# Optimization experiments

Hardware: AMD Instinct MI355X
Metric: run time of the kernel (lower is better)

Reference implementation:

```python
import jax, jax.numpy as jnp
import numpy as np

N = 100000   # nodes
E = 1600000  # edges
IN, HID, OUT = 128, 256, 64


def _glorot(key, shape):
    fan_in, fan_out = shape[1], shape[0]
    lim = (6.0 / (fan_in + fan_out)) ** 0.5
    return jax.random.uniform(key, shape, jnp.float32, -lim, lim)


def setup_inputs() -> dict:
    key = jax.random.key(0)
    ks = jax.random.split(key, 8)
    x = jax.random.normal(ks[0], (N, IN), jnp.float32)
    edge_index = jax.random.randint(ks[1], (2, E), 0, N, jnp.int64)
    # SAGEConv params: lin_l (neighbor path, has bias), lin_r (root path, no bias)
    return {
        "x": x,
        "edge_index": edge_index,
        "W1_l": _glorot(ks[2], (HID, IN)),
        "b1": jnp.zeros((HID,), jnp.float32),
        "W1_r": _glorot(ks[3], (HID, IN)),
        "W2_l": _glorot(ks[4], (OUT, HID)),
        "b2": jnp.zeros((OUT,), jnp.float32),
        "W2_r": _glorot(ks[5], (OUT, HID)),
    }


def _sage_conv(x, src, dst, W_l, b, W_r):
    # mean aggregation of neighbor features at destination nodes
    msg = x[src]                                             # [E, d] gather
    agg = jax.ops.segment_sum(msg, dst, num_segments=N)      # [N, d]
    cnt = jax.ops.segment_sum(jnp.ones((src.shape[0],), jnp.float32), dst,
                              num_segments=N)                # [N]
    mean = agg / jnp.maximum(cnt, 1.0)[:, None]
    return mean @ W_l.T + b + x @ W_r.T


def reference(x, edge_index, W1_l, b1, W1_r, W2_l, b2, W2_r):
    src, dst = edge_index[0], edge_index[1]
    h = jax.nn.relu(_sage_conv(x, src, dst, W1_l, b1, W1_r))
    # dropout is identity in eval mode
    return _sage_conv(h, src, dst, W2_l, b2, W2_r)
```

## Files before the change

kernel.cpp:

```cpp
#include <hip/hip_runtime.h>
#include <hip/hip_bf16.h>

#define NNODE 100000
#define NEDGE 1600000
#define NBBLK 512
#define CHUNK (NEDGE / NBBLK)
#define NB2 ((NNODE + 1023) >> 10)

typedef __attribute__((ext_vector_type(8))) short bf16x8;
typedef __attribute__((ext_vector_type(4))) float f32x4;
typedef __attribute__((ext_vector_type(2))) float f32x2;

__device__ __forceinline__ unsigned short f2bf(float f){
  unsigned u = __float_as_uint(f);
  u += 0x7fffu + ((u >> 16) & 1u);
  return (unsigned short)(u >> 16);
}
__device__ __forceinline__ unsigned pk2(float a, float b){
  return (unsigned)f2bf(a) | ((unsigned)f2bf(b) << 16);
}
__device__ __forceinline__ float bflo(unsigned v){ return __uint_as_float(v << 16); }
__device__ __forceinline__ float bfhi(unsigned v){ return __uint_as_float(v & 0xffff0000u); }

__global__ __launch_bounds__(256) void k_hist(const int* __restrict__ dst,
                                              unsigned* __restrict__ gh){
  __shared__ unsigned h[NB2];
  for (int t = threadIdx.x; t < NB2; t += 256) h[t] = 0;
  __syncthreads();
  int base = blockIdx.x * CHUNK;
  for (int j = threadIdx.x; j < CHUNK; j += 256)
    atomicAdd(&h[dst[base + j] >> 10], 1u);
  __syncthreads();
  for (int t = threadIdx.x; t < NB2; t += 256) gh[blockIdx.x * NB2 + t] = h[t];
}

__global__ __launch_bounds__(512) void k_scan512(const unsigned* __restrict__ gh,
                                                 unsigned* __restrict__ gbase,
                                                 unsigned* __restrict__ btot){
  int b = blockIdx.x, t = threadIdx.x;
  int lane = t & 63, wv = t >> 6;
  unsigned v = gh[t * NB2 + b];
  unsigned s = v;
  #pragma unroll
  for (int off = 1; off < 64; off <<= 1){
    unsigned u = __shfl_up(s, off, 64);
    if (lane >= off) s += u;
  }
  __shared__ unsigned wsum[8];
  if (lane == 63) wsum[wv] = s;
  __syncthreads();
  unsigned woff = 0;
  for (int w = 0; w < wv; ++w) woff += wsum[w];
  gbase[t * NB2 + b] = woff + s - v;
  if (t == 511) btot[b] = woff + s;
}

__global__ __launch_bounds__(128) void k_scanb(const unsigned* __restrict__ btot,
                                               unsigned* __restrict__ bbase,
                                               unsigned* __restrict__ rowptr){
  __shared__ unsigned buf[128];
  int tid = threadIdx.x;
  unsigned v = (tid < NB2) ? btot[tid] : 0u;
  buf[tid] = v;
  __syncthreads();
  #pragma unroll
  for (int off = 1; off < 128; off <<= 1){
    unsigned t = (tid >= off) ? buf[tid - off] : 0u;
    __syncthreads();
    buf[tid] += t;
    __syncthreads();
  }
  if (tid < NB2) bbase[tid] = buf[tid] - v;
  if (tid == 0){ bbase[NB2] = NEDGE; rowptr[NNODE] = NEDGE; }
}

__global__ __launch_bounds__(256) void k_binscat(const int* __restrict__ src,
                                                 const int* __restrict__ dst,
                                                 const unsigned* __restrict__ gbase,
                                                 const unsigned* __restrict__ bbase,
                                                 unsigned* __restrict__ pairs){
  __shared__ unsigned cur[NB2];
  for (int t = threadIdx.x; t < NB2; t += 256)
    cur[t] = bbase[t] + gbase[blockIdx.x * NB2 + t];
  __syncthreads();
  int base = blockIdx.x * CHUNK;
  for (int j = threadIdx.x; j < CHUNK; j += 256){
    int s = src[base + j], d = dst[base + j];
    unsigned p = atomicAdd(&cur[d >> 10], 1u);
    pairs[p] = ((unsigned)s << 10) | (unsigned)(d & 1023);
  }
}

__global__ __launch_bounds__(1024) void k_buildcsr(const unsigned* __restrict__ bbase,
                                                   const unsigned* __restrict__ pairs,
                                                   unsigned* __restrict__ rowptr,
                                                   unsigned* __restrict__ col){
  __shared__ unsigned hist[1024];
  __shared__ unsigned wsum[16];
  const int b = blockIdx.x, tid = threadIdx.x;
  const int lane = tid & 63, wv = tid >> 6;
  const unsigned e0 = bbase[b], e1 = bbase[b + 1];
  const int nb0 = b << 10;
  hist[tid] = 0;
  __syncthreads();
  for (unsigned j = e0 + tid; j < e1; j += 1024)
    atomicAdd(&hist[pairs[j] & 1023u], 1u);
  __syncthreads();
  unsigned v = hist[tid];
  unsigned s = v;
  #pragma unroll
  for (int off = 1; off < 64; off <<= 1){
    unsigned u = __shfl_up(s, off, 64);
    if (lane >= off) s += u;
  }
  if (lane == 63) wsum[wv] = s;
  __syncthreads();
  unsigned woff = 0;
  for (int w = 0; w < wv; ++w) woff += wsum[w];
  unsigned gpos = e0 + woff + s - v;
  if (nb0 + tid < NNODE) rowptr[nb0 + tid] = gpos;
  __syncthreads();
  hist[tid] = gpos;
  __syncthreads();
  for (unsigned j = e0 + tid; j < e1; j += 1024){
    unsigned e = pairs[j];
    unsigned p = atomicAdd(&hist[e & 1023u], 1u);
    col[p] = e >> 10;
  }
}

__global__ void k_xcvt(const float* __restrict__ x, unsigned* __restrict__ A1u,
                       unsigned* __restrict__ x8u){
  int i = blockIdx.x * 256 + threadIdx.x;
  if (i >= NNODE * 32) return;
  float4 v = ((const float4*)x)[i];
  int e = i * 4;
  int row = e >> 7, c = e & 127;
  unsigned* d = A1u + (size_t)row * 128 + 64 + (c >> 1);
  d[0] = pk2(v.x, v.y);
  d[1] = pk2(v.z, v.w);
  unsigned p = (unsigned)__builtin_amdgcn_cvt_pk_fp8_f32(v.x, v.y, 0, false);
  p = (unsigned)__builtin_amdgcn_cvt_pk_fp8_f32(v.z, v.w, (int)p, true);
  x8u[(size_t)row * 32 + (c >> 2)] = p;
}

__global__ void k_wcvt1(const float* __restrict__ W1l, const float* __restrict__ W1r,
                        unsigned short* __restrict__ Bwt1){
  int i = blockIdx.x * 256 + threadIdx.x;
  if (i >= 256 * 256) return;
  int n = i >> 8, k = i & 255;
  float v = (k < 128) ? W1l[n * 128 + k] : W1r[n * 128 + (k - 128)];
  Bwt1[i] = f2bf(v);
}

__global__ void k_wcvt2(const float* __restrict__ W2l, const float* __restrict__ W2r,
                        unsigned short* __restrict__ Bwt2){
  int i = blockIdx.x * 256 + threadIdx.x;
  if (i >= 128 * 256) return;
  int n = i >> 8, k = i & 255;
  float v = (n < 64) ? W2l[n * 256 + k] : W2r[(n - 64) * 256 + k];
  Bwt2[i] = f2bf(v);
}

__global__ void k_zcvt(const unsigned* __restrict__ zru, unsigned* __restrict__ z8u){
  int i = blockIdx.x * 256 + threadIdx.x;
  if (i >= NNODE * 16) return;
  int node = i >> 4, g = i & 15;
  uint2 v = ((const uint2*)(zru + (size_t)node * 64))[g];
  unsigned p = (unsigned)__builtin_amdgcn_cvt_pk_fp8_f32(bflo(v.x), bfhi(v.x), 0, false);
  p = (unsigned)__builtin_amdgcn_cvt_pk_fp8_f32(bflo(v.y), bfhi(v.y), (int)p, true);
  z8u[(size_t)node * 16 + g] = p;
}

__global__ __launch_bounds__(256) void k_agg1(const unsigned* __restrict__ rowptr,
                                              const unsigned* __restrict__ col,
                                              const unsigned* __restrict__ x8u,
                                              unsigned* __restrict__ A1u){
  int gw = (blockIdx.x * 256 + threadIdx.x) >> 6;
  int lane = threadIdx.x & 63;
  if (gw >= NNODE) return;
  unsigned s0 = rowptr[gw], s1 = rowptr[gw + 1];
  const int sel = lane >> 4, u = lane & 15;
  const uint2* x82 = (const uint2*)x8u;
  float a0=0.f,a1=0.f,a2=0.f,a3=0.f,a4=0.f,a5=0.f,a6=0.f,a7=0.f;
  unsigned j = s0;
  for (; j + 7 < s1; j += 8){
    unsigned ca = col[j + sel], cb = col[j + 4 + sel];
    uint2 va = x82[(size_t)ca * 16 + u];
    uint2 vb = x82[(size_t)cb * 16 + u];
    f32x2 p;
    p = __builtin_amdgcn_cvt_pk_f32_fp8((int)va.x, false); a0+=p.x; a1+=p.y;
    p = __builtin_amdgcn_cvt_pk_f32_fp8((int)va.x, true ); a2+=p.x; a3+=p.y;
    p = __builtin_amdgcn_cvt_pk_f32_fp8((int)va.y, false); a4+=p.x; a5+=p.y;
    p = __builtin_amdgcn_cvt_pk_f32_fp8((int)va.y, true ); a6+=p.x; a7+=p.y;
    p = __builtin_amdgcn_cvt_pk_f32_fp8((int)vb.x, false); a0+=p.x; a1+=p.y;
    p = __builtin_amdgcn_cvt_pk_f32_fp8((int)vb.x, true ); a2+=p.x; a3+=p.y;
    p = __builtin_amdgcn_cvt_pk_f32_fp8((int)vb.y, false); a4+=p.x; a5+=p.y;
    p = __builtin_amdgcn_cvt_pk_f32_fp8((int)vb.y, true ); a6+=p.x; a7+=p.y;
  }
  for (; j + 3 < s1; j += 4){
    unsigned ca = col[j + sel];
    uint2 va = x82[(size_t)ca * 16 + u];
    f32x2 p;
    p = __builtin_amdgcn_cvt_pk_f32_fp8((int)va.x, false); a0+=p.x; a1+=p.y;
    p = __builtin_amdgcn_cvt_pk_f32_fp8((int)va.x, true ); a2+=p.x; a3+=p.y;
    p = __builtin_amdgcn_cvt_pk_f32_fp8((int)va.y, false); a4+=p.x; a5+=p.y;
    p = __builtin_amdgcn_cvt_pk_f32_fp8((int)va.y, true ); a6+=p.x; a7+=p.y;
  }
  int rem = (int)(s1 - j);
  if (sel < rem){
    unsigned ca = col[j + sel];
    uint2 va = x82[(size_t)ca * 16 + u];
    f32x2 p;
    p = __builtin_amdgcn_cvt_pk_f32_fp8((int)va.x, false); a0+=p.x; a1+=p.y;
    p = __builtin_amdgcn_cvt_pk_f32_fp8((int)va.x, true ); a2+=p.x; a3+=p.y;
    p = __builtin_amdgcn_cvt_pk_f32_fp8((int)va.y, false); a4+=p.x; a5+=p.y;
    p = __builtin_amdgcn_cvt_pk_f32_fp8((int)va.y, true ); a6+=p.x; a7+=p.y;
  }
  a0 += __shfl_xor(a0, 16, 64); a1 += __shfl_xor(a1, 16, 64);
  a2 += __shfl_xor(a2, 16, 64); a3 += __shfl_xor(a3, 16, 64);
  a4 += __shfl_xor(a4, 16, 64); a5 += __shfl_xor(a5, 16, 64);
  a6 += __shfl_xor(a6, 16, 64); a7 += __shfl_xor(a7, 16, 64);
  a0 += __shfl_xor(a0, 32, 64); a1 += __shfl_xor(a1, 32, 64);
  a2 += __shfl_xor(a2, 32, 64); a3 += __shfl_xor(a3, 32, 64);
  a4 += __shfl_xor(a4, 32, 64); a5 += __shfl_xor(a5, 32, 64);
  a6 += __shfl_xor(a6, 32, 64); a7 += __shfl_xor(a7, 32, 64);
  if (lane < 16){
    float inv = 1.f / fmaxf((float)(s1 - s0), 1.f);
    uint4 w;
    w.x = pk2(a0 * inv, a1 * inv);
    w.y = pk2(a2 * inv, a3 * inv);
    w.z = pk2(a4 * inv, a5 * inv);
    w.w = pk2(a6 * inv, a7 * inv);
    *(uint4*)(A1u + (size_t)gw * 128 + 4 * lane) = w;
  }
}

template<int BN, bool RELU, bool BIAS>
__global__ __launch_bounds__(256) void k_gemm(const unsigned short* __restrict__ A,
                                              const unsigned short* __restrict__ B,
                                              const float* __restrict__ bias,
                                              unsigned short* __restrict__ C,
                                              int nrows){
  constexpr int NF = BN / 64;
  __shared__ unsigned short a_t[64 * 64];
  __shared__ unsigned short b_t[BN * 64];
  const int tid = threadIdx.x, wave = tid >> 6, lane = tid & 63;
  const int row0 = blockIdx.x * 64;
  char* ab = (char*)a_t;
  char* bb = (char*)b_t;

  f32x4 acc[4][NF];
  #pragma unroll
  for (int m = 0; m < 4; ++m)
    #pragma unroll
    for (int n = 0; n < NF; ++n)
      acc[m][n] = (f32x4){0.f, 0.f, 0.f, 0.f};

  for (int kt = 0; kt < 4; ++kt){
    {
      int r = tid >> 2;
      int gr = row0 + r; if (gr > nrows - 1) gr = nrows - 1;
      const uint4* s4 = (const uint4*)(A + (size_t)gr * 256 + kt * 64);
      int c0 = (tid & 3) * 2;
      uint4 v0 = s4[c0], v1 = s4[c0 + 1];
      *(uint4*)(ab + r * 128 + ((c0 * 16) ^ ((r & 7) << 4))) = v0;
      *(uint4*)(ab + r * 128 + (((c0 + 1) * 16) ^ ((r & 7) << 4))) = v1;
    }
    {
      constexpr int CPT = BN / 32;
      #pragma unroll
      for (int c = 0; c < CPT; ++c){
        int gc = tid * CPT + c;
        int n = gc >> 3, ck = gc & 7;
        uint4 v = ((const uint4*)(B + (size_t)n * 256 + kt * 64))[ck];
        *(uint4*)(bb + n * 128 + ((ck * 16) ^ ((n & 7) << 4))) = v;
      }
    }
    __syncthreads();
    #pragma unroll
    for (int kk = 0; kk < 2; ++kk){
      int k2 = (kk * 32 + ((lane >> 4) * 8)) * 2;
      bf16x8 af[4];
      #pragma unroll
      for (int m = 0; m < 4; ++m){
        int rr = m * 16 + (lane & 15);
        af[m] = *(const bf16x8*)(ab + rr * 128 + (k2 ^ ((rr & 7) << 4)));
      }
      #pragma unroll
      for (int n = 0; n < NF; ++n){
        int cc = wave * (16 * NF) + n * 16 + (lane & 15);
        bf16x8 bfv = *(const bf16x8*)(bb + cc * 128 + (k2 ^ ((cc & 7) << 4)));
        #pragma unroll
        for (int m = 0; m < 4; ++m)
          acc[m][n] = __builtin_amdgcn_mfma_f32_16x16x32_bf16(af[m], bfv, acc[m][n], 0, 0, 0);
      }
    }
    __syncthreads();
  }
  #pragma unroll
  for (int m = 0; m < 4; ++m){
    int rbase = row0 + m * 16 + ((lane >> 4) << 2);
    #pragma unroll
    for (int r = 0; r < 4; ++r){
      if (rbase + r < nrows){
        #pragma unroll
        for (int n = 0; n < NF; ++n){
          int cc = wave * (16 * NF) + n * 16 + (lane & 15);
          float v = acc[m][n][r];
          if (BIAS) v += bias[cc];
          if (RELU) v = fmaxf(v, 0.f);
          C[(size_t)(rbase + r) * BN + cc] = f2bf(v);
        }
      }
    }
  }
}

__global__ __launch_bounds__(256) void k_agg2(const unsigned* __restrict__ rowptr,
                                              const unsigned* __restrict__ col,
                                              const unsigned* __restrict__ z8u,
                                              const unsigned* __restrict__ zru,
                                              const float* __restrict__ b2,
                                              float* __restrict__ out){
  int gw = (blockIdx.x * 256 + threadIdx.x) >> 6;
  int lane = threadIdx.x & 63;
  if (gw >= NNODE) return;
  unsigned s0 = rowptr[gw], s1 = rowptr[gw + 1];
  const int sel = lane >> 4, u = lane & 15;
  float a0=0.f,a1=0.f,a2=0.f,a3=0.f;
  unsigned j = s0;
  for (; j + 7 < s1; j += 8){
    unsigned ca = col[j + sel], cb = col[j + 4 + sel];
    unsigned va = z8u[(size_t)ca * 16 + u];
    unsigned vb = z8u[(size_t)cb * 16 + u];
    f32x2 p;
    p = __builtin_amdgcn_cvt_pk_f32_fp8((int)va, false); a0+=p.x; a1+=p.y;
    p = __builtin_amdgcn_cvt_pk_f32_fp8((int)va, true ); a2+=p.x; a3+=p.y;
    p = __builtin_amdgcn_cvt_pk_f32_fp8((int)vb, false); a0+=p.x; a1+=p.y;
    p = __builtin_amdgcn_cvt_pk_f32_fp8((int)vb, true ); a2+=p.x; a3+=p.y;
  }
  for (; j + 3 < s1; j += 4){
    unsigned ca = col[j + sel];
    unsigned va = z8u[(size_t)ca * 16 + u];
    f32x2 p;
    p = __builtin_amdgcn_cvt_pk_f32_fp8((int)va, false); a0+=p.x; a1+=p.y;
    p = __builtin_amdgcn_cvt_pk_f32_fp8((int)va, true ); a2+=p.x; a3+=p.y;
  }
  int rem = (int)(s1 - j);
  if (sel < rem){
    unsigned ca = col[j + sel];
    unsigned va = z8u[(size_t)ca * 16 + u];
    f32x2 p;
    p = __builtin_amdgcn_cvt_pk_f32_fp8((int)va, false); a0+=p.x; a1+=p.y;
    p = __builtin_amdgcn_cvt_pk_f32_fp8((int)va, true ); a2+=p.x; a3+=p.y;
  }
  a0 += __shfl_xor(a0, 16, 64); a1 += __shfl_xor(a1, 16, 64);
  a2 += __shfl_xor(a2, 16, 64); a3 += __shfl_xor(a3, 16, 64);
  a0 += __shfl_xor(a0, 32, 64); a1 += __shfl_xor(a1, 32, 64);
  a2 += __shfl_xor(a2, 32, 64); a3 += __shfl_xor(a3, 32, 64);
  if (lane < 16){
    float inv = 1.f / fmaxf((float)(s1 - s0), 1.f);
    uint2 rv = ((const uint2*)(zru + (size_t)gw * 64 + 32))[lane];
    float4 bv = ((const float4*)b2)[lane];
    float4 res;
    res.x = a0 * inv + bflo(rv.x) + bv.x;
    res.y = a1 * inv + bfhi(rv.x) + bv.y;
    res.z = a2 * inv + bflo(rv.y) + bv.z;
    res.w = a3 * inv + bfhi(rv.y) + bv.w;
    ((float4*)out)[(size_t)gw * 16 + lane] = res;
  }
}

extern "C" void kernel_launch(void* const* d_in, const int* in_sizes, int n_in,
                              void* d_out, int out_size, void* d_ws, size_t ws_size,
                              hipStream_t stream) {
  const float* x   = (const float*)d_in[0];
  const int*   ei  = (const int*)d_in[1];
  const float* W1l = (const float*)d_in[2];
  const float* b1  = (const float*)d_in[3];
  const float* W1r = (const float*)d_in[4];
  const float* W2l = (const float*)d_in[5];
  const float* b2  = (const float*)d_in[6];
  const float* W2r = (const float*)d_in[7];
  float* out = (float*)d_out;

  char* ws = (char*)d_ws;
  size_t off = 0;
  auto alloc = [&](size_t bytes) -> void* {
    void* p = ws + off;
    off = (off + bytes + 255) & ~(size_t)255;
    return p;
  };
  unsigned* rowptr = (unsigned*)alloc((size_t)(NNODE + 1) * 4);
  unsigned* col    = (unsigned*)alloc((size_t)NEDGE * 4);
  unsigned* pairs  = (unsigned*)alloc((size_t)NEDGE * 4);
  unsigned* gh     = (unsigned*)alloc((size_t)NBBLK * NB2 * 4);
  unsigned* gbase  = (unsigned*)alloc((size_t)NBBLK * NB2 * 4);
  unsigned* btot   = (unsigned*)alloc((size_t)NB2 * 4);
  unsigned* bbase  = (unsigned*)alloc((size_t)(NB2 + 1) * 4);
  unsigned short* A1   = (unsigned short*)alloc((size_t)NNODE * 256 * 2);
  unsigned short* h    = (unsigned short*)alloc((size_t)NNODE * 256 * 2);
  unsigned short* zr   = (unsigned short*)alloc((size_t)NNODE * 128 * 2);
  unsigned* x8u        = (unsigned*)alloc((size_t)NNODE * 32 * 4);
  unsigned* z8u        = (unsigned*)alloc((size_t)NNODE * 16 * 4);
  unsigned short* Bwt1 = (unsigned short*)alloc(256 * 256 * 2);
  unsigned short* Bwt2 = (unsigned short*)alloc(128 * 256 * 2);

  const int* srcv = ei;
  const int* dstv = ei + NEDGE;

  k_hist<<<NBBLK, 256, 0, stream>>>(dstv, gh);
  k_scan512<<<NB2, 512, 0, stream>>>(gh, gbase, btot);
  k_scanb<<<1, 128, 0, stream>>>(btot, bbase, rowptr);
  k_binscat<<<NBBLK, 256, 0, stream>>>(srcv, dstv, gbase, bbase, pairs);
  k_buildcsr<<<NB2, 1024, 0, stream>>>(bbase, pairs, rowptr, col);

  k_xcvt<<<(NNODE * 32 + 255) / 256, 256, 0, stream>>>(x, (unsigned*)A1, x8u);
  k_wcvt1<<<256, 256, 0, stream>>>(W1l, W1r, Bwt1);
  k_wcvt2<<<128, 256, 0, stream>>>(W2l, W2r, Bwt2);

  k_agg1<<<(NNODE + 3) / 4, 256, 0, stream>>>(rowptr, col, x8u, (unsigned*)A1);

  int gblocks = (NNODE + 63) / 64;
  k_gemm<256, true,  true ><<<gblocks, 256, 0, stream>>>(A1, Bwt1, b1, h, NNODE);
  k_gemm<128, false, false><<<gblocks, 256, 0, stream>>>(h,  Bwt2, nullptr, zr, NNODE);

  k_zcvt<<<(NNODE * 16 + 255) / 256, 256, 0, stream>>>((const unsigned*)zr, z8u);
  k_agg2<<<(NNODE + 3) / 4, 256, 0, stream>>>(rowptr, col, z8u, (const unsigned*)zr, b2, out);
}
```

Measured before the change: 324.8 us.

## Fuse histogram with x conversion, merge weight casts, fold fp8 cast into GEMM2

Merges the dst histogram and the x bf16/fp8 conversion into one launch, and merges the two weight-conversion kernels into one. The second GEMM now writes fp8 neighbor-path outputs and bf16 root-path outputs directly, which removes the separate z conversion kernel and its extra read and write of z. Both aggregation loops are unrolled to 16 edges per iteration to keep more gathers in flight. The GEMM epilogue now does scattered byte stores for fp8, which may be less efficient, and the deeper unroll raises register use.

After: 314.2 us. 3.3% less time.

```diff
diff --git a/kernel.cpp b/kernel.cpp
--- a/kernel.cpp
+++ b/kernel.cpp
@@ -22,16 +22,34 @@
 __device__ __forceinline__ float bflo(unsigned v){ return __uint_as_float(v << 16); }
 __device__ __forceinline__ float bfhi(unsigned v){ return __uint_as_float(v & 0xffff0000u); }
 
-__global__ __launch_bounds__(256) void k_hist(const int* __restrict__ dst,
-                                              unsigned* __restrict__ gh){
-  __shared__ unsigned h[NB2];
-  for (int t = threadIdx.x; t < NB2; t += 256) h[t] = 0;
-  __syncthreads();
-  int base = blockIdx.x * CHUNK;
-  for (int j = threadIdx.x; j < CHUNK; j += 256)
-    atomicAdd(&h[dst[base + j] >> 10], 1u);
-  __syncthreads();
-  for (int t = threadIdx.x; t < NB2; t += 256) gh[blockIdx.x * NB2 + t] = h[t];
+__global__ __launch_bounds__(256) void k_xh(const float* __restrict__ x,
+                                            unsigned* __restrict__ A1u,
+                                            unsigned* __restrict__ x8u,
+                                            const int* __restrict__ dst,
+                                            unsigned* __restrict__ gh){
+  int bid = blockIdx.x;
+  if (bid < NBBLK){
+    __shared__ unsigned h[NB2];
+    for (int t = threadIdx.x; t < NB2; t += 256) h[t] = 0;
+    __syncthreads();
+    int base = bid * CHUNK;
+    for (int j = threadIdx.x; j < CHUNK; j += 256)
+      atomicAdd(&h[dst[base + j] >> 10], 1u);
+    __syncthreads();
+    for (int t = threadIdx.x; t < NB2; t += 256) gh[bid * NB2 + t] = h[t];
+    return;
+  }
+  int i = (bid - NBBLK) * 256 + threadIdx.x;
+  if (i >= NNODE * 32) return;
+  float4 v = ((const float4*)x)[i];
+  int e = i * 4;
+  int row = e >> 7, c = e & 127;
+  unsigned* d = A1u + (size_t)row * 128 + 64 + (c >> 1);
+  d[0] = pk2(v.x, v.y);
+  d[1] = pk2(v.z, v.w);
+  unsigned p = (unsigned)__builtin_amdgcn_cvt_pk_fp8_f32(v.x, v.y, 0, false);
+  p = (unsigned)__builtin_amdgcn_cvt_pk_fp8_f32(v.z, v.w, (int)p, true);
+  x8u[(size_t)row * 32 + (c >> 2)] = p;
 }
 
 __global__ __launch_bounds__(512) void k_scan512(const unsigned* __restrict__ gh,
@@ -129,47 +147,21 @@
   }
 }
 
-__global__ void k_xcvt(const float* __restrict__ x, unsigned* __restrict__ A1u,
-                       unsigned* __restrict__ x8u){
+__global__ void k_wcvt(const float* __restrict__ W1l, const float* __restrict__ W1r,
+                       const float* __restrict__ W2l, const float* __restrict__ W2r,
+                       unsigned short* __restrict__ Bwt1, unsigned short* __restrict__ Bwt2){
   int i = blockIdx.x * 256 + threadIdx.x;
-  if (i >= NNODE * 32) return;
-  float4 v = ((const float4*)x)[i];
-  int e = i * 4;
-  int row = e >> 7, c = e & 127;
-  unsigned* d = A1u + (size_t)row * 128 + 64 + (c >> 1);
-  d[0] = pk2(v.x, v.y);
-  d[1] = pk2(v.z, v.w);
-  unsigned p = (unsigned)__builtin_amdgcn_cvt_pk_fp8_f32(v.x, v.y, 0, false);
-  p = (unsigned)__builtin_amdgcn_cvt_pk_fp8_f32(v.z, v.w, (int)p, true);
-  x8u[(size_t)row * 32 + (c >> 2)] = p;
-}
-
-__global__ void k_wcvt1(const float* __restrict__ W1l, const float* __restrict__ W1r,
-                        unsigned short* __restrict__ Bwt1){
-  int i = blockIdx.x * 256 + threadIdx.x;
-  if (i >= 256 * 256) return;
-  int n = i >> 8, k = i & 255;
-  float v = (k < 128) ? W1l[n * 128 + k] : W1r[n * 128 + (k - 128)];
-  Bwt1[i] = f2bf(v);
-}
-
-__global__ void k_wcvt2(const float* __restrict__ W2l, const float* __restrict__ W2r,
-                        unsigned short* __restrict__ Bwt2){
-  int i = blockIdx.x * 256 + threadIdx.x;
-  if (i >= 128 * 256) return;
-  int n = i >> 8, k = i & 255;
-  float v = (n < 64) ? W2l[n * 256 + k] : W2r[(n - 64) * 256 + k];
-  Bwt2[i] = f2bf(v);
-}
-
-__global__ void k_zcvt(const unsigned* __restrict__ zru, unsigned* __restrict__ z8u){
-  int i = blockIdx.x * 256 + threadIdx.x;
-  if (i >= NNODE * 16) return;
-  int node = i >> 4, g = i & 15;
-  uint2 v = ((const uint2*)(zru + (size_t)node * 64))[g];
-  unsigned p = (unsigned)__builtin_amdgcn_cvt_pk_fp8_f32(bflo(v.x), bfhi(v.x), 0, false);
-  p = (unsigned)__builtin_amdgcn_cvt_pk_fp8_f32(bflo(v.y), bfhi(v.y), (int)p, true);
-  z8u[(size_t)node * 16 + g] = p;
+  if (i < 256 * 256){
+    int n = i >> 8, k = i & 255;
+    float v = (k < 128) ? W1l[n * 128 + k] : W1r[n * 128 + (k - 128)];
+    Bwt1[i] = f2bf(v);
+  }
+  int i2 = i - 256 * 256;
+  if (i2 >= 0 && i2 < 128 * 256){
+    int n = i2 >> 8, k = i2 & 255;
+    float v = (n < 64) ? W2l[n * 256 + k] : W2r[(n - 64) * 256 + k];
+    Bwt2[i2] = f2bf(v);
+  }
 }
 
 __global__ __launch_bounds__(256) void k_agg1(const unsigned* __restrict__ rowptr,
@@ -183,12 +175,15 @@
   const int sel = lane >> 4, u = lane & 15;
   const uint2* x82 = (const uint2*)x8u;
   float a0=0.f,a1=0.f,a2=0.f,a3=0.f,a4=0.f,a5=0.f,a6=0.f,a7=0.f;
+  f32x2 p;
   unsigned j = s0;
-  for (; j + 7 < s1; j += 8){
+  for (; j + 15 < s1; j += 16){
     unsigned ca = col[j + sel], cb = col[j + 4 + sel];
+    unsigned cc = col[j + 8 + sel], cd = col[j + 12 + sel];
     uint2 va = x82[(size_t)ca * 16 + u];
     uint2 vb = x82[(size_t)cb * 16 + u];
-    f32x2 p;
+    uint2 vc = x82[(size_t)cc * 16 + u];
+    uint2 vd = x82[(size_t)cd * 16 + u];
     p = __builtin_amdgcn_cvt_pk_f32_fp8((int)va.x, false); a0+=p.x; a1+=p.y;
     p = __builtin_amdgcn_cvt_pk_f32_fp8((int)va.x, true ); a2+=p.x; a3+=p.y;
     p = __builtin_amdgcn_cvt_pk_f32_fp8((int)va.y, false); a4+=p.x; a5+=p.y;
@@ -197,11 +192,18 @@
     p = __builtin_amdgcn_cvt_pk_f32_fp8((int)vb.x, true ); a2+=p.x; a3+=p.y;
     p = __builtin_amdgcn_cvt_pk_f32_fp8((int)vb.y, false); a4+=p.x; a5+=p.y;
     p = __builtin_amdgcn_cvt_pk_f32_fp8((int)vb.y, true ); a6+=p.x; a7+=p.y;
+    p = __builtin_amdgcn_cvt_pk_f32_fp8((int)vc.x, false); a0+=p.x; a1+=p.y;
+    p = __builtin_amdgcn_cvt_pk_f32_fp8((int)vc.x, true ); a2+=p.x; a3+=p.y;
+    p = __builtin_amdgcn_cvt_pk_f32_fp8((int)vc.y, false); a4+=p.x; a5+=p.y;
+    p = __builtin_amdgcn_cvt_pk_f32_fp8((int)vc.y, true ); a6+=p.x; a7+=p.y;
+    p = __builtin_amdgcn_cvt_pk_f32_fp8((int)vd.x, false); a0+=p.x; a1+=p.y;
+    p = __builtin_amdgcn_cvt_pk_f32_fp8((int)vd.x, true ); a2+=p.x; a3+=p.y;
+    p = __builtin_amdgcn_cvt_pk_f32_fp8((int)vd.y, false); a4+=p.x; a5+=p.y;
+    p = __builtin_amdgcn_cvt_pk_f32_fp8((int)vd.y, true ); a6+=p.x; a7+=p.y;
   }
   for (; j + 3 < s1; j += 4){
     unsigned ca = col[j + sel];
     uint2 va = x82[(size_t)ca * 16 + u];
-    f32x2 p;
     p = __builtin_amdgcn_cvt_pk_f32_fp8((int)va.x, false); a0+=p.x; a1+=p.y;
     p = __builtin_amdgcn_cvt_pk_f32_fp8((int)va.x, true ); a2+=p.x; a3+=p.y;
     p = __builtin_amdgcn_cvt_pk_f32_fp8((int)va.y, false); a4+=p.x; a5+=p.y;
@@ -211,7 +213,6 @@
   if (sel < rem){
     unsigned ca = col[j + sel];
     uint2 va = x82[(size_t)ca * 16 + u];
-    f32x2 p;
     p = __builtin_amdgcn_cvt_pk_f32_fp8((int)va.x, false); a0+=p.x; a1+=p.y;
     p = __builtin_amdgcn_cvt_pk_f32_fp8((int)va.x, true ); a2+=p.x; a3+=p.y;
     p = __builtin_amdgcn_cvt_pk_f32_fp8((int)va.y, false); a4+=p.x; a5+=p.y;
@@ -236,11 +237,13 @@
   }
 }
 
-template<int BN, bool RELU, bool BIAS>
+template<int BN, bool RELU, bool BIAS, int MODE>
 __global__ __launch_bounds__(256) void k_gemm(const unsigned short* __restrict__ A,
                                               const unsigned short* __restrict__ B,
                                               const float* __restrict__ bias,
                                               unsigned short* __restrict__ C,
+                                              unsigned char* __restrict__ z8,
+                                              unsigned short* __restrict__ r16,
                                               int nrows){
   constexpr int NF = BN / 64;
   __shared__ unsigned short a_t[64 * 64];
@@ -310,7 +313,15 @@
           float v = acc[m][n][r];
           if (BIAS) v += bias[cc];
           if (RELU) v = fmaxf(v, 0.f);
-          C[(size_t)(rbase + r) * BN + cc] = f2bf(v);
+          if (MODE == 0){
+            C[(size_t)(rbase + r) * BN + cc] = f2bf(v);
+          } else {
+            if (cc < 64)
+              z8[(size_t)(rbase + r) * 64 + cc] =
+                (unsigned char)__builtin_amdgcn_cvt_pk_fp8_f32(v, v, 0, false);
+            else
+              r16[(size_t)(rbase + r) * 64 + (cc - 64)] = f2bf(v);
+          }
         }
       }
     }
@@ -320,7 +331,7 @@
 __global__ __launch_bounds__(256) void k_agg2(const unsigned* __restrict__ rowptr,
                                               const unsigned* __restrict__ col,
                                               const unsigned* __restrict__ z8u,
-                                              const unsigned* __restrict__ zru,
+                                              const unsigned* __restrict__ r16u,
                                               const float* __restrict__ b2,
                                               float* __restrict__ out){
   int gw = (blockIdx.x * 256 + threadIdx.x) >> 6;
@@ -329,21 +340,27 @@
   unsigned s0 = rowptr[gw], s1 = rowptr[gw + 1];
   const int sel = lane >> 4, u = lane & 15;
   float a0=0.f,a1=0.f,a2=0.f,a3=0.f;
+  f32x2 p;
   unsigned j = s0;
-  for (; j + 7 < s1; j += 8){
+  for (; j + 15 < s1; j += 16){
     unsigned ca = col[j + sel], cb = col[j + 4 + sel];
+    unsigned cc = col[j + 8 + sel], cd = col[j + 12 + sel];
     unsigned va = z8u[(size_t)ca * 16 + u];
     unsigned vb = z8u[(size_t)cb * 16 + u];
-    f32x2 p;
+    unsigned vc = z8u[(size_t)cc * 16 + u];
+    unsigned vd = z8u[(size_t)cd * 16 + u];
     p = __builtin_amdgcn_cvt_pk_f32_fp8((int)va, false); a0+=p.x; a1+=p.y;
     p = __builtin_amdgcn_cvt_pk_f32_fp8((int)va, true ); a2+=p.x; a3+=p.y;
     p = __builtin_amdgcn_cvt_pk_f32_fp8((int)vb, false); a0+=p.x; a1+=p.y;
     p = __builtin_amdgcn_cvt_pk_f32_fp8((int)vb, true ); a2+=p.x; a3+=p.y;
+    p = __builtin_amdgcn_cvt_pk_f32_fp8((int)vc, false); a0+=p.x; a1+=p.y;
+    p = __builtin_amdgcn_cvt_pk_f32_fp8((int)vc, true ); a2+=p.x; a3+=p.y;
+    p = __builtin_amdgcn_cvt_pk_f32_fp8((int)vd, false); a0+=p.x; a1+=p.y;
+    p = __builtin_amdgcn_cvt_pk_f32_fp8((int)vd, true ); a2+=p.x; a3+=p.y;
   }
   for (; j + 3 < s1; j += 4){
     unsigned ca = col[j + sel];
     unsigned va = z8u[(size_t)ca * 16 + u];
-    f32x2 p;
     p = __builtin_amdgcn_cvt_pk_f32_fp8((int)va, false); a0+=p.x; a1+=p.y;
     p = __builtin_amdgcn_cvt_pk_f32_fp8((int)va, true ); a2+=p.x; a3+=p.y;
   }
@@ -351,7 +368,6 @@
   if (sel < rem){
     unsigned ca = col[j + sel];
     unsigned va = z8u[(size_t)ca * 16 + u];
-    f32x2 p;
     p = __builtin_amdgcn_cvt_pk_f32_fp8((int)va, false); a0+=p.x; a1+=p.y;
     p = __builtin_amdgcn_cvt_pk_f32_fp8((int)va, true ); a2+=p.x; a3+=p.y;
   }
@@ -361,7 +377,7 @@
   a2 += __shfl_xor(a2, 32, 64); a3 += __shfl_xor(a3, 32, 64);
   if (lane < 16){
     float inv = 1.f / fmaxf((float)(s1 - s0), 1.f);
-    uint2 rv = ((const uint2*)(zru + (size_t)gw * 64 + 32))[lane];
+    uint2 rv = ((const uint2*)(r16u + (size_t)gw * 32))[lane];
     float4 bv = ((const float4*)b2)[lane];
     float4 res;
     res.x = a0 * inv + bflo(rv.x) + bv.x;
@@ -401,31 +417,28 @@
   unsigned* bbase  = (unsigned*)alloc((size_t)(NB2 + 1) * 4);
   unsigned short* A1   = (unsigned short*)alloc((size_t)NNODE * 256 * 2);
   unsigned short* h    = (unsigned short*)alloc((size_t)NNODE * 256 * 2);
-  unsigned short* zr   = (unsigned short*)alloc((size_t)NNODE * 128 * 2);
+  unsigned short* r16  = (unsigned short*)alloc((size_t)NNODE * 64 * 2);
   unsigned* x8u        = (unsigned*)alloc((size_t)NNODE * 32 * 4);
-  unsigned* z8u        = (unsigned*)alloc((size_t)NNODE * 16 * 4);
+  unsigned char* z8    = (unsigned char*)alloc((size_t)NNODE * 64);
   unsigned short* Bwt1 = (unsigned short*)alloc(256 * 256 * 2);
   unsigned short* Bwt2 = (unsigned short*)alloc(128 * 256 * 2);
 
   const int* srcv = ei;
   const int* dstv = ei + NEDGE;
 
-  k_hist<<<NBBLK, 256, 0, stream>>>(dstv, gh);
+  k_xh<<<NBBLK + (NNODE * 32 + 255) / 256, 256, 0, stream>>>(x, (unsigned*)A1, x8u, dstv, gh);
   k_scan512<<<NB2, 512, 0, stream>>>(gh, gbase, btot);
   k_scanb<<<1, 128, 0, stream>>>(btot, bbase, rowptr);
   k_binscat<<<NBBLK, 256, 0, stream>>>(srcv, dstv, gbase, bbase, pairs);
   k_buildcsr<<<NB2, 1024, 0, stream>>>(bbase, pairs, rowptr, col);
 
-  k_xcvt<<<(NNODE * 32 + 255) / 256, 256, 0, stream>>>(x, (unsigned*)A1, x8u);
-  k_wcvt1<<<256, 256, 0, stream>>>(W1l, W1r, Bwt1);
-  k_wcvt2<<<128, 256, 0, stream>>>(W2l, W2r, Bwt2);
+  k_wcvt<<<(256 * 256 + 128 * 256 + 255) / 256, 256, 0, stream>>>(W1l, W1r, W2l, W2r, Bwt1, Bwt2);
 
   k_agg1<<<(NNODE + 3) / 4, 256, 0, stream>>>(rowptr, col, x8u, (unsigned*)A1);
 
   int gblocks = (NNODE + 63) / 64;
-  k_gemm<256, true,  true ><<<gblocks, 256, 0, stream>>>(A1, Bwt1, b1, h, NNODE);
-  k_gemm<128, false, false><<<gblocks, 256, 0, stream>>>(h,  Bwt2, nullptr, zr, NNODE);
-
-  k_zcvt<<<(NNODE * 16 + 255) / 256, 256, 0, stream>>>((const unsigned*)zr, z8u);
-  k_agg2<<<(NNODE + 3) / 4, 256, 0, stream>>>(rowptr, col, z8u, (const unsigned*)zr, b2, out);
-}
+  k_gemm<256, true,  true,  0><<<gblocks, 256, 0, stream>>>(A1, Bwt1, b1, h, nullptr, nullptr, NNODE);
+  k_gemm<128, false, false, 2><<<gblocks, 256, 0, stream>>>(h,  Bwt2, nullptr, nullptr, z8, r16, NNODE);
+
+  k_agg2<<<(NNODE + 3) / 4, 256, 0, stream>>>(rowptr, col, (const unsigned*)z8, (const unsigned*)r16, b2, out);
+}
```
